# Optimization experiments

Hardware: AMD Instinct MI355X
Metric: run time of the kernel (lower is better)

The kernel has to match this reference:

```python
import jax, jax.numpy as jnp
import numpy as np

NUM_EMBEDDINGS = 1024
EMBEDDING_DIM = 64


def setup_inputs() -> dict:
    key = jax.random.key(0)
    k1, k2 = jax.random.split(key)
    z = jax.random.normal(k1, (64, 32, 32, EMBEDDING_DIM), dtype=jnp.float32)
    # torch init: uniform_(-1/num_embeddings, 1/num_embeddings)
    lim = 1.0 / NUM_EMBEDDINGS
    codebook = jax.random.uniform(
        k2, (NUM_EMBEDDINGS, EMBEDDING_DIM), dtype=jnp.float32,
        minval=-lim, maxval=lim)
    return {"z": z, "codebook": codebook}


def reference(z, codebook):
    # z: [..., D]; codebook: [K, D]
    z_flat = z.reshape(-1, z.shape[-1])                      # [N, D]
    # ||z||^2 - 2 z.e + ||e||^2  -> [N, K]
    distances = (
        jnp.sum(z_flat ** 2, axis=1, keepdims=True)
        - 2.0 * jnp.einsum("nd,kd->nk", z_flat, codebook)
        + jnp.sum(codebook ** 2, axis=1)
    )
    min_indices = jnp.argmin(distances, axis=1)              # [N]
    z_q = jnp.take(codebook, min_indices, axis=0).reshape(z.shape)
    return z_q, min_indices
```

## Files before the change

kernel.cpp:

```cpp
#include <hip/hip_runtime.h>
#include <hip/hip_bf16.h>
#include <math.h>


#define D      64
#define K      1024
#define BLOCK  256

typedef _Float16 half8_t __attribute__((ext_vector_type(8)));
typedef float    floatx4 __attribute__((ext_vector_type(4)));

#define WS_CN_OFF    0
#define WS_EF_OFF    4096

__device__ __forceinline__ float np_sumsq64_p(const float* __restrict__ x) {
    float r[8];
    {
        float4 v0 = *(const float4*)(x);
        float4 v1 = *(const float4*)(x + 4);
        r[0] = __fmul_rn(v0.x, v0.x); r[1] = __fmul_rn(v0.y, v0.y);
        r[2] = __fmul_rn(v0.z, v0.z); r[3] = __fmul_rn(v0.w, v0.w);
        r[4] = __fmul_rn(v1.x, v1.x); r[5] = __fmul_rn(v1.y, v1.y);
        r[6] = __fmul_rn(v1.z, v1.z); r[7] = __fmul_rn(v1.w, v1.w);
    }
#pragma unroll
    for (int i = 8; i < 64; i += 8) {
        float4 v0 = *(const float4*)(x + i);
        float4 v1 = *(const float4*)(x + i + 4);
        r[0] = __fadd_rn(r[0], __fmul_rn(v0.x, v0.x));
        r[1] = __fadd_rn(r[1], __fmul_rn(v0.y, v0.y));
        r[2] = __fadd_rn(r[2], __fmul_rn(v0.z, v0.z));
        r[3] = __fadd_rn(r[3], __fmul_rn(v0.w, v0.w));
        r[4] = __fadd_rn(r[4], __fmul_rn(v1.x, v1.x));
        r[5] = __fadd_rn(r[5], __fmul_rn(v1.y, v1.y));
        r[6] = __fadd_rn(r[6], __fmul_rn(v1.z, v1.z));
        r[7] = __fadd_rn(r[7], __fmul_rn(v1.w, v1.w));
    }
    return __fadd_rn(__fadd_rn(__fadd_rn(r[0], r[1]), __fadd_rn(r[2], r[3])),
                     __fadd_rn(__fadd_rn(r[4], r[5]), __fadd_rn(r[6], r[7])));
}

__global__ void vq_pre(const float* __restrict__ cb, float* __restrict__ cn,
                       _Float16* __restrict__ ef) {
    const int k = blockIdx.x * 64 + threadIdx.x;
    if (k >= K) return;
    cn[k] = np_sumsq64_p(cb + (long)k * D);
    const int t = k >> 6, ct = (k >> 4) & 3, l16 = k & 15;
#pragma unroll
    for (int ch = 0; ch < 2; ++ch)
#pragma unroll
        for (int quad = 0; quad < 4; ++quad) {
            const float* p = cb + (long)k * D + ch * 32 + quad * 8;
            half8_t h1, h2;
#pragma unroll
            for (int j = 0; j < 8; ++j) {
                float x10 = __fmul_rn(p[j], 1024.0f);
                _Float16 g1 = (_Float16)x10;
                h1[j] = g1;
                h2[j] = (_Float16)(__fmul_rn(__fsub_rn(x10, (float)g1), 2048.0f));
            }
            const int base = t * 8192 + ct * 2048 + 128 * quad + 8 * l16;
            *(half8_t*)(ef + base + 512 * (ch))       = h1;
            *(half8_t*)(ef + base + 512 * (2 + ch))   = h2;
        }
}

__global__ __launch_bounds__(BLOCK, 2) void vq_main(
    const float* __restrict__ z, const float* __restrict__ cb,
    const _Float16* __restrict__ ef, const float* __restrict__ cn,
    float* __restrict__ zq, float* __restrict__ idx_out) {
    __shared__ __align__(16) float zf[128 * 68];
    __shared__ float sS[128];
    __shared__ float sCn[K];
    __shared__ int   sBi[128];

    const int tid  = threadIdx.x;
    const int lane = tid & 63;
    const int wv   = tid >> 6;
    const int quad = lane >> 4;
    const int l16  = lane & 15;
    const long rowbase = (long)blockIdx.x * 128;

    const float4* gz = (const float4*)(z + rowbase * D);
#pragma unroll
    for (int i = 0; i < 8; ++i) {
        int idx4 = i * BLOCK + tid;
        int r = idx4 >> 4, j = idx4 & 15;
        *(float4*)(zf + r * 68 + j * 4) = gz[idx4];
    }
#pragma unroll
    for (int i = 0; i < 4; ++i) sCn[i * 256 + tid] = cn[i * 256 + tid];
    __syncthreads();

    if (tid < 128) sS[tid] = np_sumsq64_p(zf + tid * 68);

    half8_t a1[2][2], a2[2][2];
#pragma unroll
    for (int rt = 0; rt < 2; ++rt) {
        const int row = wv * 32 + rt * 16 + l16;
#pragma unroll
        for (int ch = 0; ch < 2; ++ch) {
            const float* p = zf + row * 68 + ch * 32 + quad * 8;
            float4 f0 = *(const float4*)(p);
            float4 f1 = *(const float4*)(p + 4);
            float xs[8] = {f0.x, f0.y, f0.z, f0.w, f1.x, f1.y, f1.z, f1.w};
#pragma unroll
            for (int j = 0; j < 8; ++j) {
                _Float16 h1 = (_Float16)xs[j];
                a1[rt][ch][j] = h1;
                a2[rt][ch][j] =
                    (_Float16)(__fmul_rn(__fsub_rn(xs[j], (float)h1), 2048.0f));
            }
        }
    }
    __syncthreads();

    float myS[2][4];
#pragma unroll
    for (int rt = 0; rt < 2; ++rt)
#pragma unroll
        for (int r = 0; r < 4; ++r)
            myS[rt][r] = sS[wv * 32 + rt * 16 + quad * 4 + r];

    float bv[2][4];
    int   bi[2][4];
#pragma unroll
    for (int rt = 0; rt < 2; ++rt)
#pragma unroll
        for (int r = 0; r < 4; ++r) { bv[rt][r] = INFINITY; bi[rt][r] = 0; }

    const char* eb = (const char*)ef + 16 * lane;

#define LOADG(b1_, b2_, g_) do {                                              \
        const char* p_ = eb + (size_t)(g_) * 4096;                            \
        b1_[0] = *(const half8_t*)(p_);                                       \
        b1_[1] = *(const half8_t*)(p_ + 1024);                                \
        b2_[0] = *(const half8_t*)(p_ + 2048);                                \
        b2_[1] = *(const half8_t*)(p_ + 3072);                                \
    } while (0)

#define COMPUTE(b1_, b2_, g_) do {                                            \
        const int   kg_  = (g_) * 16 + l16;                                   \
        const float cnv_ = sCn[kg_];                                          \
        const floatx4 Z4_ = {0.f, 0.f, 0.f, 0.f};                             \
        floatx4 aM0, aM1, aC0, aC1;                                           \
        aM0 = __builtin_amdgcn_mfma_f32_16x16x32_f16(a1[0][0], b1_[0], Z4_, 0, 0, 0); \
        aM1 = __builtin_amdgcn_mfma_f32_16x16x32_f16(a1[1][0], b1_[0], Z4_, 0, 0, 0); \
        aM0 = __builtin_amdgcn_mfma_f32_16x16x32_f16(a1[0][1], b1_[1], aM0, 0, 0, 0); \
        aM1 = __builtin_amdgcn_mfma_f32_16x16x32_f16(a1[1][1], b1_[1], aM1, 0, 0, 0); \
        aC0 = __builtin_amdgcn_mfma_f32_16x16x32_f16(a1[0][0], b2_[0], Z4_, 0, 0, 0); \
        aC1 = __builtin_amdgcn_mfma_f32_16x16x32_f16(a1[1][0], b2_[0], Z4_, 0, 0, 0); \
        aC0 = __builtin_amdgcn_mfma_f32_16x16x32_f16(a1[0][1], b2_[1], aC0, 0, 0, 0); \
        aC1 = __builtin_amdgcn_mfma_f32_16x16x32_f16(a1[1][1], b2_[1], aC1, 0, 0, 0); \
        aC0 = __builtin_amdgcn_mfma_f32_16x16x32_f16(a2[0][0], b1_[0], aC0, 0, 0, 0); \
        aC1 = __builtin_amdgcn_mfma_f32_16x16x32_f16(a2[1][0], b1_[0], aC1, 0, 0, 0); \
        aC0 = __builtin_amdgcn_mfma_f32_16x16x32_f16(a2[0][1], b1_[1], aC0, 0, 0, 0); \
        aC1 = __builtin_amdgcn_mfma_f32_16x16x32_f16(a2[1][1], b1_[1], aC1, 0, 0, 0); \
        _Pragma("unroll")                                                     \
        for (int r = 0; r < 4; ++r) {                                         \
            float ds0 = fmaf(aC0[r], 0x1p-11f, aM0[r]);                       \
            float d0  = __fadd_rn(__fsub_rn(myS[0][r],                        \
                            __fmul_rn(ds0, 0x1p-9f)), cnv_);                  \
            if (d0 < bv[0][r]) { bv[0][r] = d0; bi[0][r] = kg_; }             \
            float ds1 = fmaf(aC1[r], 0x1p-11f, aM1[r]);                       \
            float d1  = __fadd_rn(__fsub_rn(myS[1][r],                        \
                            __fmul_rn(ds1, 0x1p-9f)), cnv_);                  \
            if (d1 < bv[1][r]) { bv[1][r] = d1; bi[1][r] = kg_; }             \
        }                                                                     \
    } while (0)

    half8_t b1A[2], b2A[2], b1B[2], b2B[2];
    LOADG(b1A, b2A, 0);
    for (int g = 0; g < 64; g += 2) {
        LOADG(b1B, b2B, g + 1);
        COMPUTE(b1A, b2A, g);
        if (g < 62) LOADG(b1A, b2A, g + 2);
        COMPUTE(b1B, b2B, g + 1);
    }

#undef LOADG
#undef COMPUTE

#pragma unroll
    for (int rt = 0; rt < 2; ++rt)
#pragma unroll
        for (int r = 0; r < 4; ++r) {
            float v = bv[rt][r];
            int   x = bi[rt][r];
#pragma unroll
            for (int off = 1; off <= 8; off <<= 1) {
                float ov = __shfl_xor(v, off);
                int   ox = __shfl_xor(x, off);
                if (ov < v || (ov == v && ox < x)) { v = ov; x = ox; }
            }
            if (l16 == 0) {
                const int rl = wv * 32 + rt * 16 + quad * 4 + r;
                sBi[rl] = x;
                idx_out[rowbase + rl] = (float)x;
            }
        }
    __syncthreads();

    const float4* cb4 = (const float4*)cb;
    float4* zq4 = (float4*)(zq + rowbase * D);
#pragma unroll
    for (int i = 0; i < 8; ++i) {
        int idx4 = i * BLOCK + tid;
        int r = idx4 >> 4, j = idx4 & 15;
        zq4[idx4] = cb4[(long)sBi[r] * 16 + j];
    }
}

extern "C" void kernel_launch(void* const* d_in, const int* in_sizes, int n_in,
                              void* d_out, int out_size, void* d_ws, size_t ws_size,
                              hipStream_t stream) {
    const float* z  = (const float*)d_in[0];
    const float* cb = (const float*)d_in[1];

    const int n_rows = in_sizes[0] / D;
    float* zq      = (float*)d_out;
    float* idx_out = zq + (long)n_rows * D;

    float*    ws_cn = (float*)((char*)d_ws + WS_CN_OFF);
    _Float16* ws_ef = (_Float16*)((char*)d_ws + WS_EF_OFF);

    vq_pre<<<K / 64, 64, 0, stream>>>(cb, ws_cn, ws_ef);
    vq_main<<<n_rows / 128, BLOCK, 0, stream>>>(z, cb, ws_ef, ws_cn, zq, idx_out);
}
```

Baseline: 102.0 us.

## Switch distance GEMM to 32x32x16 MFMA with matching codebook layout and prescaled norms

Replaces the paired 16x16x32 f16 MFMA tiles with single 32x32x16 MFMA tiles per wave and rewrites the codebook preprocessing layout to match the new B-operand fragment order. The row and codebook norms are prescaled by 512, which removes a multiply from the per-element epilogue. The goal is fewer MFMA issues and a cheaper epilogue per codebook group. In exchange the accumulators grow to 16 floats per thread, raising register pressure, and the argmin shuffle reduction now spans 32 lanes.

```diff
diff --git a/kernel.cpp b/kernel.cpp
--- a/kernel.cpp
+++ b/kernel.cpp
@@ -7,8 +7,8 @@
 #define K      1024
 #define BLOCK  256
 
-typedef _Float16 half8_t __attribute__((ext_vector_type(8)));
-typedef float    floatx4 __attribute__((ext_vector_type(4)));
+typedef _Float16 half8_t  __attribute__((ext_vector_type(8)));
+typedef float    floatx16 __attribute__((ext_vector_type(16)));
 
 #define WS_CN_OFF    0
 #define WS_EF_OFF    4096
@@ -45,12 +45,12 @@
     const int k = blockIdx.x * 64 + threadIdx.x;
     if (k >= K) return;
     cn[k] = np_sumsq64_p(cb + (long)k * D);
-    const int t = k >> 6, ct = (k >> 4) & 3, l16 = k & 15;
-#pragma unroll
-    for (int ch = 0; ch < 2; ++ch)
-#pragma unroll
-        for (int quad = 0; quad < 4; ++quad) {
-            const float* p = cb + (long)k * D + ch * 32 + quad * 8;
+    const int g = k >> 5, c32 = k & 31;
+#pragma unroll
+    for (int ks = 0; ks < 4; ++ks)
+#pragma unroll
+        for (int hi = 0; hi < 2; ++hi) {
+            const float* p = cb + (long)k * D + ks * 16 + hi * 8;
             half8_t h1, h2;
 #pragma unroll
             for (int j = 0; j < 8; ++j) {
@@ -59,9 +59,9 @@
                 h1[j] = g1;
                 h2[j] = (_Float16)(__fmul_rn(__fsub_rn(x10, (float)g1), 2048.0f));
             }
-            const int base = t * 8192 + ct * 2048 + 128 * quad + 8 * l16;
-            *(half8_t*)(ef + base + 512 * (ch))       = h1;
-            *(half8_t*)(ef + base + 512 * (2 + ch))   = h2;
+            const int base = g * 4096 + (hi * 32 + c32) * 8;
+            *(half8_t*)(ef + base + ks * 512)       = h1;
+            *(half8_t*)(ef + base + (4 + ks) * 512) = h2;
         }
 }
 
@@ -77,8 +77,8 @@
     const int tid  = threadIdx.x;
     const int lane = tid & 63;
     const int wv   = tid >> 6;
-    const int quad = lane >> 4;
-    const int l16  = lane & 15;
+    const int c32  = lane & 31;
+    const int hi   = lane >> 5;
     const long rowbase = (long)blockIdx.x * 128;
 
     const float4* gz = (const float4*)(z + rowbase * D);
@@ -89,116 +89,111 @@
         *(float4*)(zf + r * 68 + j * 4) = gz[idx4];
     }
 #pragma unroll
-    for (int i = 0; i < 4; ++i) sCn[i * 256 + tid] = cn[i * 256 + tid];
+    for (int i = 0; i < 4; ++i)
+        sCn[i * 256 + tid] = __fmul_rn(cn[i * 256 + tid], 512.0f);
     __syncthreads();
 
-    if (tid < 128) sS[tid] = np_sumsq64_p(zf + tid * 68);
-
-    half8_t a1[2][2], a2[2][2];
-#pragma unroll
-    for (int rt = 0; rt < 2; ++rt) {
-        const int row = wv * 32 + rt * 16 + l16;
-#pragma unroll
-        for (int ch = 0; ch < 2; ++ch) {
-            const float* p = zf + row * 68 + ch * 32 + quad * 8;
+    if (tid < 128) sS[tid] = __fmul_rn(np_sumsq64_p(zf + tid * 68), 512.0f);
+
+    half8_t a1[4], a2[4];
+    {
+        const int arow = wv * 32 + c32;
+#pragma unroll
+        for (int ks = 0; ks < 4; ++ks) {
+            const float* p = zf + arow * 68 + ks * 16 + hi * 8;
             float4 f0 = *(const float4*)(p);
             float4 f1 = *(const float4*)(p + 4);
             float xs[8] = {f0.x, f0.y, f0.z, f0.w, f1.x, f1.y, f1.z, f1.w};
 #pragma unroll
             for (int j = 0; j < 8; ++j) {
                 _Float16 h1 = (_Float16)xs[j];
-                a1[rt][ch][j] = h1;
-                a2[rt][ch][j] =
+                a1[ks][j] = h1;
+                a2[ks][j] =
                     (_Float16)(__fmul_rn(__fsub_rn(xs[j], (float)h1), 2048.0f));
             }
         }
     }
     __syncthreads();
 
-    float myS[2][4];
-#pragma unroll
-    for (int rt = 0; rt < 2; ++rt)
-#pragma unroll
-        for (int r = 0; r < 4; ++r)
-            myS[rt][r] = sS[wv * 32 + rt * 16 + quad * 4 + r];
-
-    float bv[2][4];
-    int   bi[2][4];
-#pragma unroll
-    for (int rt = 0; rt < 2; ++rt)
-#pragma unroll
-        for (int r = 0; r < 4; ++r) { bv[rt][r] = INFINITY; bi[rt][r] = 0; }
+    float myS9[16];
+#pragma unroll
+    for (int r = 0; r < 16; ++r)
+        myS9[r] = sS[wv * 32 + (r & 3) + 8 * (r >> 2) + 4 * hi];
+
+    float bv[16];
+    int   bi[16];
+#pragma unroll
+    for (int r = 0; r < 16; ++r) { bv[r] = INFINITY; bi[r] = 0; }
 
     const char* eb = (const char*)ef + 16 * lane;
-
-#define LOADG(b1_, b2_, g_) do {                                              \
-        const char* p_ = eb + (size_t)(g_) * 4096;                            \
+    const floatx16 Z16 = {0.f, 0.f, 0.f, 0.f, 0.f, 0.f, 0.f, 0.f,
+                          0.f, 0.f, 0.f, 0.f, 0.f, 0.f, 0.f, 0.f};
+
+#define LOADG(b1_, b2_, cn9_, g_) do {                                        \
+        const char* p_ = eb + (size_t)(g_) * 8192;                            \
         b1_[0] = *(const half8_t*)(p_);                                       \
         b1_[1] = *(const half8_t*)(p_ + 1024);                                \
-        b2_[0] = *(const half8_t*)(p_ + 2048);                                \
-        b2_[1] = *(const half8_t*)(p_ + 3072);                                \
+        b1_[2] = *(const half8_t*)(p_ + 2048);                                \
+        b1_[3] = *(const half8_t*)(p_ + 3072);                                \
+        b2_[0] = *(const half8_t*)(p_ + 4096);                                \
+        b2_[1] = *(const half8_t*)(p_ + 5120);                                \
+        b2_[2] = *(const half8_t*)(p_ + 6144);                                \
+        b2_[3] = *(const half8_t*)(p_ + 7168);                                \
+        cn9_ = sCn[(g_) * 32 + c32];                                          \
     } while (0)
 
-#define COMPUTE(b1_, b2_, g_) do {                                            \
-        const int   kg_  = (g_) * 16 + l16;                                   \
-        const float cnv_ = sCn[kg_];                                          \
-        const floatx4 Z4_ = {0.f, 0.f, 0.f, 0.f};                             \
-        floatx4 aM0, aM1, aC0, aC1;                                           \
-        aM0 = __builtin_amdgcn_mfma_f32_16x16x32_f16(a1[0][0], b1_[0], Z4_, 0, 0, 0); \
-        aM1 = __builtin_amdgcn_mfma_f32_16x16x32_f16(a1[1][0], b1_[0], Z4_, 0, 0, 0); \
-        aM0 = __builtin_amdgcn_mfma_f32_16x16x32_f16(a1[0][1], b1_[1], aM0, 0, 0, 0); \
-        aM1 = __builtin_amdgcn_mfma_f32_16x16x32_f16(a1[1][1], b1_[1], aM1, 0, 0, 0); \
-        aC0 = __builtin_amdgcn_mfma_f32_16x16x32_f16(a1[0][0], b2_[0], Z4_, 0, 0, 0); \
-        aC1 = __builtin_amdgcn_mfma_f32_16x16x32_f16(a1[1][0], b2_[0], Z4_, 0, 0, 0); \
-        aC0 = __builtin_amdgcn_mfma_f32_16x16x32_f16(a1[0][1], b2_[1], aC0, 0, 0, 0); \
-        aC1 = __builtin_amdgcn_mfma_f32_16x16x32_f16(a1[1][1], b2_[1], aC1, 0, 0, 0); \
-        aC0 = __builtin_amdgcn_mfma_f32_16x16x32_f16(a2[0][0], b1_[0], aC0, 0, 0, 0); \
-        aC1 = __builtin_amdgcn_mfma_f32_16x16x32_f16(a2[1][0], b1_[0], aC1, 0, 0, 0); \
-        aC0 = __builtin_amdgcn_mfma_f32_16x16x32_f16(a2[0][1], b1_[1], aC0, 0, 0, 0); \
-        aC1 = __builtin_amdgcn_mfma_f32_16x16x32_f16(a2[1][1], b1_[1], aC1, 0, 0, 0); \
+#define COMPUTE(b1_, b2_, cn9_, g_) do {                                      \
+        const int kg_ = (g_) * 32 + c32;                                      \
+        floatx16 aM, aC;                                                      \
+        aM = __builtin_amdgcn_mfma_f32_32x32x16_f16(a1[0], b1_[0], Z16, 0, 0, 0); \
+        aC = __builtin_amdgcn_mfma_f32_32x32x16_f16(a1[0], b2_[0], Z16, 0, 0, 0); \
+        aM = __builtin_amdgcn_mfma_f32_32x32x16_f16(a1[1], b1_[1], aM, 0, 0, 0);  \
+        aC = __builtin_amdgcn_mfma_f32_32x32x16_f16(a1[1], b2_[1], aC, 0, 0, 0);  \
+        aM = __builtin_amdgcn_mfma_f32_32x32x16_f16(a1[2], b1_[2], aM, 0, 0, 0);  \
+        aC = __builtin_amdgcn_mfma_f32_32x32x16_f16(a1[2], b2_[2], aC, 0, 0, 0);  \
+        aM = __builtin_amdgcn_mfma_f32_32x32x16_f16(a1[3], b1_[3], aM, 0, 0, 0);  \
+        aC = __builtin_amdgcn_mfma_f32_32x32x16_f16(a1[3], b2_[3], aC, 0, 0, 0);  \
+        aC = __builtin_amdgcn_mfma_f32_32x32x16_f16(a2[0], b1_[0], aC, 0, 0, 0);  \
+        aC = __builtin_amdgcn_mfma_f32_32x32x16_f16(a2[1], b1_[1], aC, 0, 0, 0);  \
+        aC = __builtin_amdgcn_mfma_f32_32x32x16_f16(a2[2], b1_[2], aC, 0, 0, 0);  \
+        aC = __builtin_amdgcn_mfma_f32_32x32x16_f16(a2[3], b1_[3], aC, 0, 0, 0);  \
         _Pragma("unroll")                                                     \
-        for (int r = 0; r < 4; ++r) {                                         \
-            float ds0 = fmaf(aC0[r], 0x1p-11f, aM0[r]);                       \
-            float d0  = __fadd_rn(__fsub_rn(myS[0][r],                        \
-                            __fmul_rn(ds0, 0x1p-9f)), cnv_);                  \
-            if (d0 < bv[0][r]) { bv[0][r] = d0; bi[0][r] = kg_; }             \
-            float ds1 = fmaf(aC1[r], 0x1p-11f, aM1[r]);                       \
-            float d1  = __fadd_rn(__fsub_rn(myS[1][r],                        \
-                            __fmul_rn(ds1, 0x1p-9f)), cnv_);                  \
-            if (d1 < bv[1][r]) { bv[1][r] = d1; bi[1][r] = kg_; }             \
+        for (int r = 0; r < 16; ++r) {                                        \
+            float ds = fmaf(aC[r], 0x1p-11f, aM[r]);                          \
+            float d9 = __fadd_rn(__fsub_rn(myS9[r], ds), cn9_);               \
+            if (d9 < bv[r]) { bv[r] = d9; bi[r] = kg_; }                      \
         }                                                                     \
     } while (0)
 
-    half8_t b1A[2], b2A[2], b1B[2], b2B[2];
-    LOADG(b1A, b2A, 0);
-    for (int g = 0; g < 64; g += 2) {
-        LOADG(b1B, b2B, g + 1);
-        COMPUTE(b1A, b2A, g);
-        if (g < 62) LOADG(b1A, b2A, g + 2);
-        COMPUTE(b1B, b2B, g + 1);
+    half8_t b1A[4], b2A[4], b1B[4], b2B[4];
+    float cnA, cnB;
+    LOADG(b1A, b2A, cnA, 0);
+    for (int g = 0; g < 32; g += 2) {
+        LOADG(b1B, b2B, cnB, g + 1);
+        COMPUTE(b1A, b2A, cnA, g);
+        if (g + 2 < 32) LOADG(b1A, b2A, cnA, g + 2);
+        COMPUTE(b1B, b2B, cnB, g + 1);
     }
 
 #undef LOADG
 #undef COMPUTE
 
 #pragma unroll
-    for (int rt = 0; rt < 2; ++rt)
-#pragma unroll
-        for (int r = 0; r < 4; ++r) {
-            float v = bv[rt][r];
-            int   x = bi[rt][r];
-#pragma unroll
-            for (int off = 1; off <= 8; off <<= 1) {
-                float ov = __shfl_xor(v, off);
-                int   ox = __shfl_xor(x, off);
-                if (ov < v || (ov == v && ox < x)) { v = ov; x = ox; }
-            }
-            if (l16 == 0) {
-                const int rl = wv * 32 + rt * 16 + quad * 4 + r;
-                sBi[rl] = x;
-                idx_out[rowbase + rl] = (float)x;
-            }
-        }
+    for (int r = 0; r < 16; ++r) {
+        float v = bv[r];
+        int   x = bi[r];
+#pragma unroll
+        for (int off = 1; off <= 16; off <<= 1) {
+            float ov = __shfl_xor(v, off);
+            int   ox = __shfl_xor(x, off);
+            if (ov < v || (ov == v && ox < x)) { v = ov; x = ox; }
+        }
+        if (c32 == 0) {
+            const int row = wv * 32 + (r & 3) + 8 * (r >> 2) + 4 * hi;
+            sBi[row] = x;
+            idx_out[rowbase + row] = (float)x;
+        }
+    }
     __syncthreads();
 
     const float4* cb4 = (const float4*)cb;
```

Measured after the change: 107.2 us. +5.2%, slower.

## Double rows per block and prescale norms to cut per-element distance math

Applied to the files above, without the earlier changes.

Each block now handles 256 rows, so every wave covers 64 rows (4 row tiles). Each codebook fragment loaded from global memory is therefore reused across twice as many MFMAs, halving codebook traffic per row. Row and codebook norms are prescaled by 512 so the per-element multiply disappears, the codebook norm is prefetched alongside the B fragments, and the correction terms use separate accumulators. In exchange the grid is halved to 256 blocks, occupancy drops to one block per SM via launch bounds, and register pressure rises.

```diff
diff --git a/kernel.cpp b/kernel.cpp
--- a/kernel.cpp
+++ b/kernel.cpp
@@ -6,6 +6,7 @@
 #define D      64
 #define K      1024
 #define BLOCK  256
+#define ROWS   256
 
 typedef _Float16 half8_t __attribute__((ext_vector_type(8)));
 typedef float    floatx4 __attribute__((ext_vector_type(4)));
@@ -59,45 +60,57 @@
                 h1[j] = g1;
                 h2[j] = (_Float16)(__fmul_rn(__fsub_rn(x10, (float)g1), 2048.0f));
             }
-            const int base = t * 8192 + ct * 2048 + 128 * quad + 8 * l16;
+            const int base = (t * 4 + ct) * 2048 + 128 * quad + 8 * l16;
             *(half8_t*)(ef + base + 512 * (ch))       = h1;
             *(half8_t*)(ef + base + 512 * (2 + ch))   = h2;
         }
 }
 
-__global__ __launch_bounds__(BLOCK, 2) void vq_main(
+__global__ __launch_bounds__(BLOCK, 1) void vq_main(
     const float* __restrict__ z, const float* __restrict__ cb,
     const _Float16* __restrict__ ef, const float* __restrict__ cn,
     float* __restrict__ zq, float* __restrict__ idx_out) {
-    __shared__ __align__(16) float zf[128 * 68];
-    __shared__ float sS[128];
+    extern __shared__ __align__(16) float zf[];
+    __shared__ float sS[ROWS];
     __shared__ float sCn[K];
-    __shared__ int   sBi[128];
+    __shared__ int   sBi[ROWS];
 
     const int tid  = threadIdx.x;
     const int lane = tid & 63;
     const int wv   = tid >> 6;
     const int quad = lane >> 4;
     const int l16  = lane & 15;
-    const long rowbase = (long)blockIdx.x * 128;
+    const long rowbase = (long)blockIdx.x * ROWS;
+
+    const char* eb = (const char*)ef + 16 * lane;
+
+#define LOADG(b1_, b2_, cn9_, g_) do {                                        \
+        const char* p_ = eb + (size_t)(g_) * 4096;                            \
+        b1_[0] = *(const half8_t*)(p_);                                       \
+        b1_[1] = *(const half8_t*)(p_ + 1024);                                \
+        b2_[0] = *(const half8_t*)(p_ + 2048);                                \
+        b2_[1] = *(const half8_t*)(p_ + 3072);                                \
+        cn9_ = sCn[(g_) * 16 + l16];                                          \
+    } while (0)
 
     const float4* gz = (const float4*)(z + rowbase * D);
 #pragma unroll
-    for (int i = 0; i < 8; ++i) {
+    for (int i = 0; i < 16; ++i) {
         int idx4 = i * BLOCK + tid;
         int r = idx4 >> 4, j = idx4 & 15;
         *(float4*)(zf + r * 68 + j * 4) = gz[idx4];
     }
 #pragma unroll
-    for (int i = 0; i < 4; ++i) sCn[i * 256 + tid] = cn[i * 256 + tid];
+    for (int i = 0; i < 4; ++i)
+        sCn[i * 256 + tid] = __fmul_rn(cn[i * 256 + tid], 512.0f);
     __syncthreads();
 
-    if (tid < 128) sS[tid] = np_sumsq64_p(zf + tid * 68);
-
-    half8_t a1[2][2], a2[2][2];
-#pragma unroll
-    for (int rt = 0; rt < 2; ++rt) {
-        const int row = wv * 32 + rt * 16 + l16;
+    sS[tid] = __fmul_rn(np_sumsq64_p(zf + tid * 68), 512.0f);
+
+    half8_t a1[4][2], a2[4][2];
+#pragma unroll
+    for (int rt = 0; rt < 4; ++rt) {
+        const int row = wv * 64 + rt * 16 + l16;
 #pragma unroll
         for (int ch = 0; ch < 2; ++ch) {
             const float* p = zf + row * 68 + ch * 32 + quad * 8;
@@ -115,74 +128,58 @@
     }
     __syncthreads();
 
-    float myS[2][4];
-#pragma unroll
-    for (int rt = 0; rt < 2; ++rt)
+    float myS9[4][4];
+#pragma unroll
+    for (int rt = 0; rt < 4; ++rt)
 #pragma unroll
         for (int r = 0; r < 4; ++r)
-            myS[rt][r] = sS[wv * 32 + rt * 16 + quad * 4 + r];
-
-    float bv[2][4];
-    int   bi[2][4];
-#pragma unroll
-    for (int rt = 0; rt < 2; ++rt)
+            myS9[rt][r] = sS[wv * 64 + rt * 16 + quad * 4 + r];
+
+    float bv[4][4];
+    int   bi[4][4];
+#pragma unroll
+    for (int rt = 0; rt < 4; ++rt)
 #pragma unroll
         for (int r = 0; r < 4; ++r) { bv[rt][r] = INFINITY; bi[rt][r] = 0; }
 
-    const char* eb = (const char*)ef + 16 * lane;
-
-#define LOADG(b1_, b2_, g_) do {                                              \
-        const char* p_ = eb + (size_t)(g_) * 4096;                            \
-        b1_[0] = *(const half8_t*)(p_);                                       \
-        b1_[1] = *(const half8_t*)(p_ + 1024);                                \
-        b2_[0] = *(const half8_t*)(p_ + 2048);                                \
-        b2_[1] = *(const half8_t*)(p_ + 3072);                                \
-    } while (0)
-
-#define COMPUTE(b1_, b2_, g_) do {                                            \
-        const int   kg_  = (g_) * 16 + l16;                                   \
-        const float cnv_ = sCn[kg_];                                          \
-        const floatx4 Z4_ = {0.f, 0.f, 0.f, 0.f};                             \
-        floatx4 aM0, aM1, aC0, aC1;                                           \
-        aM0 = __builtin_amdgcn_mfma_f32_16x16x32_f16(a1[0][0], b1_[0], Z4_, 0, 0, 0); \
-        aM1 = __builtin_amdgcn_mfma_f32_16x16x32_f16(a1[1][0], b1_[0], Z4_, 0, 0, 0); \
-        aM0 = __builtin_amdgcn_mfma_f32_16x16x32_f16(a1[0][1], b1_[1], aM0, 0, 0, 0); \
-        aM1 = __builtin_amdgcn_mfma_f32_16x16x32_f16(a1[1][1], b1_[1], aM1, 0, 0, 0); \
-        aC0 = __builtin_amdgcn_mfma_f32_16x16x32_f16(a1[0][0], b2_[0], Z4_, 0, 0, 0); \
-        aC1 = __builtin_amdgcn_mfma_f32_16x16x32_f16(a1[1][0], b2_[0], Z4_, 0, 0, 0); \
-        aC0 = __builtin_amdgcn_mfma_f32_16x16x32_f16(a1[0][1], b2_[1], aC0, 0, 0, 0); \
-        aC1 = __builtin_amdgcn_mfma_f32_16x16x32_f16(a1[1][1], b2_[1], aC1, 0, 0, 0); \
-        aC0 = __builtin_amdgcn_mfma_f32_16x16x32_f16(a2[0][0], b1_[0], aC0, 0, 0, 0); \
-        aC1 = __builtin_amdgcn_mfma_f32_16x16x32_f16(a2[1][0], b1_[0], aC1, 0, 0, 0); \
-        aC0 = __builtin_amdgcn_mfma_f32_16x16x32_f16(a2[0][1], b1_[1], aC0, 0, 0, 0); \
-        aC1 = __builtin_amdgcn_mfma_f32_16x16x32_f16(a2[1][1], b1_[1], aC1, 0, 0, 0); \
+    const floatx4 Z4g = {0.f, 0.f, 0.f, 0.f};
+
+#define COMPUTE(b1_, b2_, cn9_, g_) do {                                      \
+        const int kg_ = (g_) * 16 + l16;                                      \
         _Pragma("unroll")                                                     \
-        for (int r = 0; r < 4; ++r) {                                         \
-            float ds0 = fmaf(aC0[r], 0x1p-11f, aM0[r]);                       \
-            float d0  = __fadd_rn(__fsub_rn(myS[0][r],                        \
-                            __fmul_rn(ds0, 0x1p-9f)), cnv_);                  \
-            if (d0 < bv[0][r]) { bv[0][r] = d0; bi[0][r] = kg_; }             \
-            float ds1 = fmaf(aC1[r], 0x1p-11f, aM1[r]);                       \
-            float d1  = __fadd_rn(__fsub_rn(myS[1][r],                        \
-                            __fmul_rn(ds1, 0x1p-9f)), cnv_);                  \
-            if (d1 < bv[1][r]) { bv[1][r] = d1; bi[1][r] = kg_; }             \
+        for (int rt = 0; rt < 4; ++rt) {                                      \
+            floatx4 aM, aC, aD;                                               \
+            aM = __builtin_amdgcn_mfma_f32_16x16x32_f16(a1[rt][0], b1_[0], Z4g, 0, 0, 0); \
+            aC = __builtin_amdgcn_mfma_f32_16x16x32_f16(a1[rt][0], b2_[0], Z4g, 0, 0, 0); \
+            aD = __builtin_amdgcn_mfma_f32_16x16x32_f16(a2[rt][0], b1_[0], Z4g, 0, 0, 0); \
+            aM = __builtin_amdgcn_mfma_f32_16x16x32_f16(a1[rt][1], b1_[1], aM, 0, 0, 0);  \
+            aC = __builtin_amdgcn_mfma_f32_16x16x32_f16(a1[rt][1], b2_[1], aC, 0, 0, 0);  \
+            aD = __builtin_amdgcn_mfma_f32_16x16x32_f16(a2[rt][1], b1_[1], aD, 0, 0, 0);  \
+            _Pragma("unroll")                                                 \
+            for (int r = 0; r < 4; ++r) {                                     \
+                float sc = __fadd_rn(aC[r], aD[r]);                           \
+                float ds = fmaf(sc, 0x1p-11f, aM[r]);                         \
+                float d9 = __fadd_rn(__fsub_rn(myS9[rt][r], ds), cn9_);       \
+                if (d9 < bv[rt][r]) { bv[rt][r] = d9; bi[rt][r] = kg_; }      \
+            }                                                                 \
         }                                                                     \
     } while (0)
 
     half8_t b1A[2], b2A[2], b1B[2], b2B[2];
-    LOADG(b1A, b2A, 0);
+    float cnA, cnB;
+    LOADG(b1A, b2A, cnA, 0);
     for (int g = 0; g < 64; g += 2) {
-        LOADG(b1B, b2B, g + 1);
-        COMPUTE(b1A, b2A, g);
-        if (g < 62) LOADG(b1A, b2A, g + 2);
-        COMPUTE(b1B, b2B, g + 1);
+        LOADG(b1B, b2B, cnB, g + 1);
+        COMPUTE(b1A, b2A, cnA, g);
+        if (g + 2 < 64) LOADG(b1A, b2A, cnA, g + 2);
+        COMPUTE(b1B, b2B, cnB, g + 1);
     }
 
 #undef LOADG
 #undef COMPUTE
 
 #pragma unroll
-    for (int rt = 0; rt < 2; ++rt)
+    for (int rt = 0; rt < 4; ++rt)
 #pragma unroll
         for (int r = 0; r < 4; ++r) {
             float v = bv[rt][r];
@@ -194,7 +191,7 @@
                 if (ov < v || (ov == v && ox < x)) { v = ov; x = ox; }
             }
             if (l16 == 0) {
-                const int rl = wv * 32 + rt * 16 + quad * 4 + r;
+                const int rl = wv * 64 + rt * 16 + quad * 4 + r;
                 sBi[rl] = x;
                 idx_out[rowbase + rl] = (float)x;
             }
@@ -204,7 +201,7 @@
     const float4* cb4 = (const float4*)cb;
     float4* zq4 = (float4*)(zq + rowbase * D);
 #pragma unroll
-    for (int i = 0; i < 8; ++i) {
+    for (int i = 0; i < 16; ++i) {
         int idx4 = i * BLOCK + tid;
         int r = idx4 >> 4, j = idx4 & 15;
         zq4[idx4] = cb4[(long)sBi[r] * 16 + j];
@@ -225,5 +222,6 @@
     _Float16* ws_ef = (_Float16*)((char*)d_ws + WS_EF_OFF);
 
     vq_pre<<<K / 64, 64, 0, stream>>>(cb, ws_cn, ws_ef);
-    vq_main<<<n_rows / 128, BLOCK, 0, stream>>>(z, cb, ws_ef, ws_cn, zq, idx_out);
-}
+    vq_main<<<n_rows / ROWS, BLOCK, ROWS * 68 * sizeof(float), stream>>>(
+        z, cb, ws_ef, ws_cn, zq, idx_out);
+}
```

Result: slower. 108.2 us (+6.1%).
